# Performance work log

Hardware: AMD Instinct MI355X
Metric: run time of the kernel (lower is better)

## Reference

```python
import jax, jax.numpy as jnp
from jax import lax
import numpy as np


def setup_inputs() -> dict:
    key = jax.random.key(0)
    ks = jax.random.split(key, 10)
    B, C, T, H, W = 4, 128, 32, 24, 24
    M, k_t, k_s, mix_k = 3, 3, 3, 3
    s = 0.05
    q = jax.random.normal(ks[0], (B, C, T, H, W), jnp.float32)
    k = jax.random.normal(ks[1], (B, C, T, H, W), jnp.float32)
    v = jax.random.normal(ks[2], (B, C, T, H, W), jnp.float32)
    # depthwise 3D kernel banks: [M, C, 1, k_t, k_s, k_s] (OIDHW per branch, groups=C)
    Wk = jax.random.normal(ks[3], (M, C, 1, k_t, k_s, k_s), jnp.float32) * s
    Wv = jax.random.normal(ks[4], (M, C, 1, k_t, k_s, k_s), jnp.float32) * s
    # mix predictor: 1x1 conv1d (pointwise) + causal conv1d C->M
    pre_w = jax.random.normal(ks[5], (C, C), jnp.float32) * s
    pre_b = jax.random.normal(ks[6], (C,), jnp.float32) * s
    mix_w = jax.random.normal(ks[7], (M, C, mix_k), jnp.float32) * s
    mix_b = jax.random.normal(ks[8], (M,), jnp.float32) * s
    return {"q": q, "k": k, "v": v, "Wk": Wk, "Wv": Wv,
            "pre_w": pre_w, "pre_b": pre_b, "mix_w": mix_w, "mix_b": mix_b}


def _mix_alpha(q, pre_w, pre_b, mix_w, mix_b):
    # q: [B,C,T,H,W] -> global spatial pool -> [B,C,T]
    qg = q.mean(axis=(3, 4))
    h = jnp.einsum('oc,bct->bot', pre_w, qg) + pre_b[None, :, None]
    h = jax.nn.gelu(h, approximate=False)  # torch nn.GELU default = exact
    mix_k = mix_w.shape[-1]
    logits = lax.conv_general_dilated(
        h, mix_w, window_strides=(1,), padding=[(mix_k - 1, 0)],
        dimension_numbers=('NCH', 'OIH', 'NCH')) + mix_b[None, :, None]
    return jax.nn.softmax(logits, axis=1)  # [B,M,T]


def _dwconv3d_causal(x, w):
    # x: [B,C,T,H,W], w: [C,1,k_t,k_h,k_w] depthwise (groups=C)
    C = x.shape[1]
    k_t, k_h, k_w = w.shape[2], w.shape[3], w.shape[4]
    pad = [(k_t - 1, 0), (k_h // 2, k_h // 2), (k_w // 2, k_w // 2)]
    return lax.conv_general_dilated(
        x, w, window_strides=(1, 1, 1), padding=pad,
        dimension_numbers=('NCDHW', 'OIDHW', 'NCDHW'),
        feature_group_count=C)


def reference(q, k, v, Wk, Wv, pre_w, pre_b, mix_w, mix_b):
    alpha = _mix_alpha(q, pre_w, pre_b, mix_w, mix_b)  # [B,M,T]
    # all M depthwise branches at once: [M,B,C,T,H,W]
    km = jax.vmap(_dwconv3d_causal, in_axes=(None, 0))(k, Wk)
    vm = jax.vmap(_dwconv3d_causal, in_axes=(None, 0))(v, Wv)
    # per-time mixture-weighted sum over M
    k_out = jnp.einsum('mbcthw,bmt->bcthw', km, alpha)
    v_out = jnp.einsum('mbcthw,bmt->bcthw', vm, alpha)
    return (k_out, v_out)
```

## Files before the change

### kernel.cpp

```cpp
#include <hip/hip_runtime.h>
#include <math.h>

namespace {
constexpr int Bn = 4, Cn = 128, Tn = 32, Hn = 24, Wn = 24, Mn = 3;
constexpr int HWn = Hn * Wn;
constexpr int TTile = 8;
constexpr int PL = TTile + 2;
constexpr int RS = 28;
constexpr int PS = 26 * RS;
}

__global__ __launch_bounds__(256) void pool_kernel(const float* __restrict__ q,
                                                   float* __restrict__ qg) {
    int wave = threadIdx.x >> 6;
    int lane = threadIdx.x & 63;
    int plane = blockIdx.x * 4 + wave;
    const float4* p = (const float4*)(q + (size_t)plane * HWn);
    float4 a = p[lane];
    float4 b = p[lane + 64];
    float s = (a.x + a.y) + (a.z + a.w) + (b.x + b.y) + (b.z + b.w);
    if (lane < 16) {
        float4 c = p[128 + lane];
        s += (c.x + c.y) + (c.z + c.w);
    }
#pragma unroll
    for (int off = 32; off > 0; off >>= 1) s += __shfl_down(s, off);
    if (lane == 0) qg[plane] = s * (1.0f / 576.0f);
}

__global__ __launch_bounds__(512) void alpha_kernel(const float* __restrict__ qg,
                                                    const float* __restrict__ pre_w,
                                                    const float* __restrict__ pre_b,
                                                    const float* __restrict__ mix_w,
                                                    const float* __restrict__ mix_b,
                                                    float* __restrict__ alpha) {
    __shared__ float qg_s[Cn * Tn];
    __shared__ float h_s[Cn * (Tn + 2)];
    __shared__ float mw_s[Mn * Cn * 3];
    __shared__ float l_s[Mn * Tn];
    int b = blockIdx.x;
    int tid = threadIdx.x;
    for (int i = tid; i < Cn * Tn; i += 512) qg_s[i] = qg[b * Cn * Tn + i];
    for (int i = tid; i < Mn * Cn * 3; i += 512) mw_s[i] = mix_w[i];
    __syncthreads();
    {
        int o = tid >> 2;
        int t0 = (tid & 3) * 8;
        float bias = pre_b[o];
        float acc[8];
#pragma unroll
        for (int j = 0; j < 8; ++j) acc[j] = 0.f;
        const float* wrow = pre_w + o * Cn;
#pragma unroll 2
        for (int cb = 0; cb < Cn; cb += 8) {
            float wv[8];
#pragma unroll
            for (int j = 0; j < 8; ++j) wv[j] = wrow[cb + j];
#pragma unroll
            for (int j = 0; j < 8; ++j)
#pragma unroll
                for (int i = 0; i < 8; ++i)
                    acc[i] += wv[j] * qg_s[(cb + j) * Tn + t0 + i];
        }
        if ((tid & 3) == 0) { h_s[o * (Tn + 2) + 0] = 0.f; h_s[o * (Tn + 2) + 1] = 0.f; }
#pragma unroll
        for (int j = 0; j < 8; ++j) {
            float x = acc[j] + bias;
            h_s[o * (Tn + 2) + 2 + t0 + j] = 0.5f * x * (1.0f + erff(x * 0.70710678118654752f));
        }
    }
    __syncthreads();
    if (tid < Mn * Tn) {
        int m = tid / Tn, t = tid % Tn;
        float acc = mix_b[m];
#pragma unroll 8
        for (int c = 0; c < Cn; ++c) {
            const float* mw = mw_s + (m * Cn + c) * 3;
            const float* hp = h_s + c * (Tn + 2) + t;
            acc += mw[0] * hp[0] + mw[1] * hp[1] + mw[2] * hp[2];
        }
        l_s[m * Tn + t] = acc;
    }
    __syncthreads();
    if (tid < Tn) {
        int t = tid;
        float l0 = l_s[t], l1 = l_s[Tn + t], l2 = l_s[2 * Tn + t];
        float mx = fmaxf(l0, fmaxf(l1, l2));
        float e0 = expf(l0 - mx), e1 = expf(l1 - mx), e2 = expf(l2 - mx);
        float inv = 1.0f / (e0 + e1 + e2);
        alpha[(b * Mn + 0) * Tn + t] = e0 * inv;
        alpha[(b * Mn + 1) * Tn + t] = e1 * inv;
        alpha[(b * Mn + 2) * Tn + t] = e2 * inv;
    }
}

__global__ __launch_bounds__(384) void conv_kernel(const float* __restrict__ kin,
                                                   const float* __restrict__ vin,
                                                   const float* __restrict__ Wk,
                                                   const float* __restrict__ Wv,
                                                   const float* __restrict__ alpha,
                                                   float* __restrict__ out) {
    __shared__ float s[PL * PS];
    __shared__ float sw[TTile * 27];

    int bid = blockIdx.x;
    int tt = bid & 3;
    int c  = (bid >> 2) & 127;
    int b  = (bid >> 9) & 3;
    int br = bid >> 11;
    int t0 = tt * TTile;
    int tid = threadIdx.x;
    const size_t plane_base = (size_t)(b * Cn + c) * Tn;
    const float* __restrict__ src = br ? vin : kin;
    const float* __restrict__ Wb  = br ? Wv : Wk;

    if (tid < PL * 26) {
        int p  = tid / 26;
        int rs = tid - p * 26;
        int tp = t0 - 2 + p;
        float4 g0, g1, g2, g3, g4, g5;
        bool valid = (tp >= 0) && ((unsigned)(rs - 1) < 24u);
        if (valid) {
            const float4* grow = (const float4*)(src + (plane_base + tp) * HWn + (rs - 1) * 24);
            g0 = grow[0]; g1 = grow[1]; g2 = grow[2];
            g3 = grow[3]; g4 = grow[4]; g5 = grow[5];
        } else {
            float4 z = make_float4(0.f, 0.f, 0.f, 0.f);
            g0 = z; g1 = z; g2 = z; g3 = z; g4 = z; g5 = z;
        }
        float4* dst = (float4*)(s + p * PS + rs * RS);
        dst[0] = make_float4(0.f,  g0.x, g0.y, g0.z);
        dst[1] = make_float4(g0.w, g1.x, g1.y, g1.z);
        dst[2] = make_float4(g1.w, g2.x, g2.y, g2.z);
        dst[3] = make_float4(g2.w, g3.x, g3.y, g3.z);
        dst[4] = make_float4(g3.w, g4.x, g4.y, g4.z);
        dst[5] = make_float4(g4.w, g5.x, g5.y, g5.z);
        dst[6] = make_float4(g5.w, 0.f,  0.f,  0.f);
    }
    if (tid < TTile * 27) {
        int tl = tid / 27;
        int widx = tid - tl * 27;
        float a0 = alpha[(b * Mn + 0) * Tn + t0 + tl];
        float a1 = alpha[(b * Mn + 1) * Tn + t0 + tl];
        float a2 = alpha[(b * Mn + 2) * Tn + t0 + tl];
        sw[tid] = a0 * Wb[(0 * Cn + c) * 27 + widx]
                + a1 * Wb[(1 * Cn + c) * 27 + widx]
                + a2 * Wb[(2 * Cn + c) * 27 + widx];
    }
    __syncthreads();

    int tl = tid / 48;
    int rem = tid - tl * 48;
    int h = rem >> 1;
    int w0 = (rem & 1) * 12;
    const float* wp = sw + tl * 27;
    float acc[12];
#pragma unroll
    for (int j = 0; j < 12; ++j) acc[j] = 0.f;
#pragma unroll
    for (int dt = 0; dt < 3; ++dt) {
#pragma unroll
        for (int dh = 0; dh < 3; ++dh) {
            const float* rp = s + (tl + dt) * PS + (h + dh) * RS + w0;
            float bf[14];
#pragma unroll
            for (int j = 0; j < 14; ++j) bf[j] = rp[j];
#pragma unroll
            for (int dw = 0; dw < 3; ++dw) {
                float wc = wp[dt * 9 + dh * 3 + dw];
#pragma unroll
                for (int j = 0; j < 12; ++j) acc[j] += bf[j + dw] * wc;
            }
        }
    }
    size_t obase = (plane_base + t0 + tl) * HWn + h * Wn + w0;
    float* op = out + (br ? (size_t)Bn * Cn * Tn * HWn : 0) + obase;
#pragma unroll
    for (int j = 0; j < 3; ++j)
        ((float4*)op)[j] = make_float4(acc[4*j], acc[4*j+1], acc[4*j+2], acc[4*j+3]);
}

extern "C" void kernel_launch(void* const* d_in, const int* in_sizes, int n_in,
                              void* d_out, int out_size, void* d_ws, size_t ws_size,
                              hipStream_t stream) {
    const float* q     = (const float*)d_in[0];
    const float* k     = (const float*)d_in[1];
    const float* v     = (const float*)d_in[2];
    const float* Wk    = (const float*)d_in[3];
    const float* Wv    = (const float*)d_in[4];
    const float* pre_w = (const float*)d_in[5];
    const float* pre_b = (const float*)d_in[6];
    const float* mix_w = (const float*)d_in[7];
    const float* mix_b = (const float*)d_in[8];
    float* out = (float*)d_out;

    float* qg    = (float*)d_ws;
    float* alpha = qg + Bn * Cn * Tn;

    hipLaunchKernelGGL(pool_kernel, dim3(Bn * Cn * Tn / 4), dim3(256), 0, stream, q, qg);
    hipLaunchKernelGGL(alpha_kernel, dim3(Bn), dim3(512), 0, stream,
                       qg, pre_w, pre_b, mix_w, mix_b, alpha);
    hipLaunchKernelGGL(conv_kernel, dim3(2 * Bn * Cn * (Tn / TTile)), dim3(384), 0, stream,
                       k, v, Wk, Wv, alpha, out);
}
```

Measured before the change: 203.5 us.

## Compute two output time steps per thread with larger time tile

```diff
diff --git a/kernel.cpp b/kernel.cpp
--- a/kernel.cpp
+++ b/kernel.cpp
@@ -4,7 +4,7 @@
 namespace {
 constexpr int Bn = 4, Cn = 128, Tn = 32, Hn = 24, Wn = 24, Mn = 3;
 constexpr int HWn = Hn * Wn;
-constexpr int TTile = 8;
+constexpr int TTile = 16;
 constexpr int PL = TTile + 2;
 constexpr int RS = 28;
 constexpr int PS = 26 * RS;
@@ -104,19 +104,19 @@
     __shared__ float sw[TTile * 27];
 
     int bid = blockIdx.x;
-    int tt = bid & 3;
-    int c  = (bid >> 2) & 127;
-    int b  = (bid >> 9) & 3;
-    int br = bid >> 11;
+    int tt = bid & 1;
+    int c  = (bid >> 1) & 127;
+    int b  = (bid >> 8) & 3;
+    int br = bid >> 10;
     int t0 = tt * TTile;
     int tid = threadIdx.x;
     const size_t plane_base = (size_t)(b * Cn + c) * Tn;
     const float* __restrict__ src = br ? vin : kin;
     const float* __restrict__ Wb  = br ? Wv : Wk;
 
-    if (tid < PL * 26) {
-        int p  = tid / 26;
-        int rs = tid - p * 26;
+    for (int idx = tid; idx < PL * 26; idx += 384) {
+        int p  = idx / 26;
+        int rs = idx - p * 26;
         int tp = t0 - 2 + p;
         float4 g0, g1, g2, g3, g4, g5;
         bool valid = (tp >= 0) && ((unsigned)(rs - 1) < 24u);
@@ -137,39 +137,52 @@
         dst[5] = make_float4(g4.w, g5.x, g5.y, g5.z);
         dst[6] = make_float4(g5.w, 0.f,  0.f,  0.f);
     }
-    if (tid < TTile * 27) {
-        int tl = tid / 27;
-        int widx = tid - tl * 27;
+    for (int i = tid; i < TTile * 27; i += 384) {
+        int tl = i / 27;
+        int widx = i - tl * 27;
         float a0 = alpha[(b * Mn + 0) * Tn + t0 + tl];
         float a1 = alpha[(b * Mn + 1) * Tn + t0 + tl];
         float a2 = alpha[(b * Mn + 2) * Tn + t0 + tl];
-        sw[tid] = a0 * Wb[(0 * Cn + c) * 27 + widx]
-                + a1 * Wb[(1 * Cn + c) * 27 + widx]
-                + a2 * Wb[(2 * Cn + c) * 27 + widx];
-    }
-    __syncthreads();
-
-    int tl = tid / 48;
-    int rem = tid - tl * 48;
+        sw[i] = a0 * Wb[(0 * Cn + c) * 27 + widx]
+              + a1 * Wb[(1 * Cn + c) * 27 + widx]
+              + a2 * Wb[(2 * Cn + c) * 27 + widx];
+    }
+    __syncthreads();
+
+    int tp8 = tid / 48;
+    int rem = tid - tp8 * 48;
     int h = rem >> 1;
     int w0 = (rem & 1) * 12;
-    const float* wp = sw + tl * 27;
-    float acc[12];
-#pragma unroll
-    for (int j = 0; j < 12; ++j) acc[j] = 0.f;
-#pragma unroll
-    for (int dt = 0; dt < 3; ++dt) {
+    int tl = tp8 * 2;
+    const float* wp0 = sw + tl * 27;
+    const float* wp1 = wp0 + 27;
+    float acc0[12], acc1[12];
+#pragma unroll
+    for (int j = 0; j < 12; ++j) { acc0[j] = 0.f; acc1[j] = 0.f; }
+#pragma unroll
+    for (int p = 0; p < 4; ++p) {
+        const float* pp = s + (tl + p) * PS;
 #pragma unroll
         for (int dh = 0; dh < 3; ++dh) {
-            const float* rp = s + (tl + dt) * PS + (h + dh) * RS + w0;
+            const float* rp = pp + (h + dh) * RS + w0;
             float bf[14];
 #pragma unroll
             for (int j = 0; j < 14; ++j) bf[j] = rp[j];
-#pragma unroll
-            for (int dw = 0; dw < 3; ++dw) {
-                float wc = wp[dt * 9 + dh * 3 + dw];
-#pragma unroll
-                for (int j = 0; j < 12; ++j) acc[j] += bf[j + dw] * wc;
+            if (p < 3) {
+#pragma unroll
+                for (int dw = 0; dw < 3; ++dw) {
+                    float wc = wp0[p * 9 + dh * 3 + dw];
+#pragma unroll
+                    for (int j = 0; j < 12; ++j) acc0[j] += bf[j + dw] * wc;
+                }
+            }
+            if (p >= 1) {
+#pragma unroll
+                for (int dw = 0; dw < 3; ++dw) {
+                    float wc = wp1[(p - 1) * 9 + dh * 3 + dw];
+#pragma unroll
+                    for (int j = 0; j < 12; ++j) acc1[j] += bf[j + dw] * wc;
+                }
             }
         }
     }
@@ -177,7 +190,11 @@
     float* op = out + (br ? (size_t)Bn * Cn * Tn * HWn : 0) + obase;
 #pragma unroll
     for (int j = 0; j < 3; ++j)
-        ((float4*)op)[j] = make_float4(acc[4*j], acc[4*j+1], acc[4*j+2], acc[4*j+3]);
+        ((float4*)op)[j] = make_float4(acc0[4*j], acc0[4*j+1], acc0[4*j+2], acc0[4*j+3]);
+    op += HWn;
+#pragma unroll
+    for (int j = 0; j < 3; ++j)
+        ((float4*)op)[j] = make_float4(acc1[4*j], acc1[4*j+1], acc1[4*j+2], acc1[4*j+3]);
 }
 
 extern "C" void kernel_launch(void* const* d_in, const int* in_sizes, int n_in,
```

After: 212.2 us. 4.3% more time.
